# Kernel tuning notes

Hardware: AMD Instinct MI355X
Metric: run time of the kernel (lower is better)

Reference implementation:

```python
import jax, jax.numpy as jnp
import numpy as np

N, E, IN, HID, HEADS, G = 50000, 800000, 300, 256, 4, 64
C1, C2, C3 = 16, 64, 256


def setup_inputs() -> dict:
    key = jax.random.key(0)
    ks = jax.random.split(key, 24)
    s = 0.05
    hd = HID // HEADS
    inp = {
        'x': jax.random.normal(ks[0], (N, IN), jnp.float32),
        'edge_index': jax.random.randint(ks[1], (2, E), 0, N, dtype=jnp.int32),
        # sorted graph ids with every segment non-empty (for global_max_pool)
        'batch': ((jnp.arange(N, dtype=jnp.int32) * G) // N).astype(jnp.int32),
        # GATConv 1: in 300 -> 4 heads x 64
        'W1': jax.random.normal(ks[2], (IN, HID), jnp.float32) * s,
        'as1': jax.random.normal(ks[3], (HEADS, hd), jnp.float32) * s,
        'ad1': jax.random.normal(ks[4], (HEADS, hd), jnp.float32) * s,
        'b1': jnp.zeros((HID,), jnp.float32),
        # GATConv 2: 256 -> 4 heads x 64
        'W2': jax.random.normal(ks[5], (HID, HID), jnp.float32) * s,
        'as2': jax.random.normal(ks[6], (HEADS, hd), jnp.float32) * s,
        'ad2': jax.random.normal(ks[7], (HEADS, hd), jnp.float32) * s,
        'b2': jnp.zeros((HID,), jnp.float32),
        # GATConv 3: 256 -> 1 head x 256
        'W3': jax.random.normal(ks[8], (HID, HID), jnp.float32) * s,
        'as3': jax.random.normal(ks[9], (1, HID), jnp.float32) * s,
        'ad3': jax.random.normal(ks[10], (1, HID), jnp.float32) * s,
        'b3': jnp.zeros((HID,), jnp.float32),
        # hierarchical classifier heads
        'Wc1': jax.random.normal(ks[11], (HID, C1), jnp.float32) * s,
        'bc1': jnp.zeros((C1,), jnp.float32),
        'Wc2': jax.random.normal(ks[12], (HID + C1, C2), jnp.float32) * s,
        'bc2': jnp.zeros((C2,), jnp.float32),
        'Wc3': jax.random.normal(ks[13], (HID + C2, C3), jnp.float32) * s,
        'bc3': jnp.zeros((C3,), jnp.float32),
    }
    return inp


def gat_conv(x, src, dst, W, a_src, a_dst, b, heads):
    """PyG-style GATConv: gather -> leaky_relu scores -> segment softmax over dst -> scatter-add."""
    n = x.shape[0]
    d = W.shape[1] // heads
    h = (x @ W).reshape(n, heads, d)                       # [N,H,D]
    alpha_s = jnp.einsum('nhd,hd->nh', h, a_src)           # [N,H]
    alpha_d = jnp.einsum('nhd,hd->nh', h, a_dst)           # [N,H]
    e = jax.nn.leaky_relu(alpha_s[src] + alpha_d[dst], 0.2)  # [E,H]
    e_max = jax.ops.segment_max(e, dst, num_segments=n)
    e_max = jnp.where(jnp.isfinite(e_max), e_max, 0.0)
    w = jnp.exp(e - e_max[dst])
    denom = jax.ops.segment_sum(w, dst, num_segments=n)
    alpha = w / (denom[dst] + 1e-16)                       # [E,H]
    out = jax.ops.segment_sum(h[src] * alpha[:, :, None], dst, num_segments=n)
    return out.reshape(n, heads * d) + b


def forward(x, edge_index, batch,
            W1, as1, ad1, b1, W2, as2, ad2, b2, W3, as3, ad3, b3,
            Wc1, bc1, Wc2, bc2, Wc3, bc3):
    n = x.shape[0]
    loop = jnp.arange(n, dtype=edge_index.dtype)           # PyG add_self_loops=True
    src = jnp.concatenate([edge_index[0], loop])
    dst = jnp.concatenate([edge_index[1], loop])
    h = jax.nn.elu(gat_conv(x, src, dst, W1, as1, ad1, b1, HEADS))
    h = jax.nn.elu(gat_conv(h, src, dst, W2, as2, ad2, b2, HEADS))  # dropout is identity in eval
    h = gat_conv(h, src, dst, W3, as3, ad3, b3, 1)
    g = jax.ops.segment_max(h, batch, num_segments=G)      # global_max_pool -> [G,HID]
    l1 = g @ Wc1 + bc1
    p1 = jax.nn.softmax(l1, axis=1)
    l2 = jnp.concatenate([g, p1], axis=1) @ Wc2 + bc2
    p2 = jax.nn.softmax(l2, axis=1)
    l3 = jnp.concatenate([g, p2], axis=1) @ Wc3 + bc3
    return (l1, l2, l3)


def reference(x, edge_index, batch,
              W1, as1, ad1, b1, W2, as2, ad2, b2, W3, as3, ad3, b3,
              Wc1, bc1, Wc2, bc2, Wc3, bc3):
    return forward(x, edge_index, batch, W1, as1, ad1, b1, W2, as2, ad2, b2,
                   W3, as3, ad3, b3, Wc1, bc1, Wc2, bc2, Wc3, bc3)
```

## Files before the change

kernel.cpp:

```cpp
#include <hip/hip_runtime.h>
#include <hip/hip_bf16.h>
#include <math.h>

#define NN 50000
#define EE 800000
#define INF_ 300
#define HIDF 256
#define GG 64

__global__ void count_dst_k(const int* __restrict__ dst, int* __restrict__ cnt, int E) {
    int e = blockIdx.x * blockDim.x + threadIdx.x;
    if (e < E) atomicAdd(&cnt[dst[e]], 1);
}

__global__ void scan1_k(const int* __restrict__ cnt, int* __restrict__ tmp,
                        int* __restrict__ bsums, int n) {
    __shared__ int sd[256];
    int t = threadIdx.x;
    int i = blockIdx.x * 256 + t;
    sd[t] = (i < n) ? cnt[i] : 0;
    __syncthreads();
    #pragma unroll
    for (int off = 1; off < 256; off <<= 1) {
        int add = (t >= off) ? sd[t - off] : 0;
        __syncthreads();
        sd[t] += add;
        __syncthreads();
    }
    if (i < n) tmp[i] = sd[t];
    if (t == 255) bsums[blockIdx.x] = sd[255];
}

__global__ void scan2_k(int* __restrict__ bsums, int nb) {
    __shared__ int sd[256];
    int t = threadIdx.x;
    sd[t] = (t < nb) ? bsums[t] : 0;
    __syncthreads();
    #pragma unroll
    for (int off = 1; off < 256; off <<= 1) {
        int add = (t >= off) ? sd[t - off] : 0;
        __syncthreads();
        sd[t] += add;
        __syncthreads();
    }
    if (t < nb) bsums[t] = sd[t];
}

__global__ void scan3_k(const int* __restrict__ tmp, const int* __restrict__ cnt,
                        const int* __restrict__ bsums, int* __restrict__ row_off,
                        int* __restrict__ wr, int n) {
    int i = blockIdx.x * 256 + threadIdx.x;
    if (i >= n) return;
    int base = (blockIdx.x > 0) ? bsums[blockIdx.x - 1] : 0;
    int incl = tmp[i] + base;
    row_off[i + 1] = incl;
    wr[i] = incl - cnt[i];
    if (i == 0) row_off[0] = 0;
}

__global__ void scatter_k(const int* __restrict__ src, const int* __restrict__ dst,
                          int* __restrict__ wr, int* __restrict__ csr_src, int E) {
    int e = blockIdx.x * blockDim.x + threadIdx.x;
    if (e < E) {
        int d = dst[e];
        int pos = atomicAdd(&wr[d], 1);
        csr_src[pos] = src[e];
    }
}

__global__ __launch_bounds__(256) void gemm_f32(const float* __restrict__ A,
                                                const float* __restrict__ B,
                                                float* __restrict__ C, int M, int K) {
    __shared__ float sA[16][64];
    __shared__ float sB[16][64];
    const int tid = threadIdx.x;
    const int tr = tid >> 4, tc = tid & 15;
    const int r0 = tr * 4, c0 = tc * 4;
    const int bm = blockIdx.x * 64;
    const int bn = blockIdx.y * 64;

    float acc[4][4] = {};

    const int aRow = tid >> 2;
    const int aK   = (tid & 3) * 4;
    const int bRow = tid >> 4;
    const int bCol = (tid & 15) * 4;
    const bool aValid = (bm + aRow) < M;
    const float* Arow = A + (size_t)(bm + aRow) * K;
    const int nK = (K + 15) >> 4;

    for (int t = 0; t < nK; ++t) {
        int k0 = t * 16;
        if (aValid && (k0 + aK + 3) < K) {
            float4 v = *(const float4*)(Arow + k0 + aK);
            sA[aK + 0][aRow] = v.x;
            sA[aK + 1][aRow] = v.y;
            sA[aK + 2][aRow] = v.z;
            sA[aK + 3][aRow] = v.w;
        } else {
            #pragma unroll
            for (int j = 0; j < 4; ++j) {
                int k = k0 + aK + j;
                sA[aK + j][aRow] = (aValid && k < K) ? Arow[k] : 0.f;
            }
        }
        {
            int k = k0 + bRow;
            float4 v = make_float4(0.f, 0.f, 0.f, 0.f);
            if (k < K) v = *(const float4*)(B + (size_t)k * 256 + bn + bCol);
            *(float4*)&sB[bRow][bCol] = v;
        }
        __syncthreads();
        #pragma unroll
        for (int k = 0; k < 16; ++k) {
            float4 a4 = *(float4*)&sA[k][r0];
            float4 b4 = *(float4*)&sB[k][c0];
            acc[0][0] += a4.x * b4.x; acc[0][1] += a4.x * b4.y; acc[0][2] += a4.x * b4.z; acc[0][3] += a4.x * b4.w;
            acc[1][0] += a4.y * b4.x; acc[1][1] += a4.y * b4.y; acc[1][2] += a4.y * b4.z; acc[1][3] += a4.y * b4.w;
            acc[2][0] += a4.z * b4.x; acc[2][1] += a4.z * b4.y; acc[2][2] += a4.z * b4.z; acc[2][3] += a4.z * b4.w;
            acc[3][0] += a4.w * b4.x; acc[3][1] += a4.w * b4.y; acc[3][2] += a4.w * b4.z; acc[3][3] += a4.w * b4.w;
        }
        __syncthreads();
    }
    #pragma unroll
    for (int i = 0; i < 4; ++i) {
        int m = bm + r0 + i;
        if (m < M) {
            float4 v = make_float4(acc[i][0], acc[i][1], acc[i][2], acc[i][3]);
            *(float4*)(C + (size_t)m * 256 + bn + c0) = v;
        }
    }
}

template <int NH>
__global__ __launch_bounds__(256) void calc_alpha_k(const float* __restrict__ hf,
                                                    const float* __restrict__ a_s,
                                                    const float* __restrict__ a_d,
                                                    float* __restrict__ als,
                                                    float* __restrict__ ald, int n) {
    int gw = (blockIdx.x * blockDim.x + threadIdx.x) >> 6;
    int lane = threadIdx.x & 63;
    if (gw >= n) return;
    const float* hr = hf + (size_t)gw * 256;
    float ps[4], pd[4];
    #pragma unroll
    for (int j = 0; j < 4; ++j) {
        float v = hr[j * 64 + lane];
        ps[j] = v * a_s[j * 64 + lane];
        pd[j] = v * a_d[j * 64 + lane];
    }
    if (NH == 1) {
        ps[0] = (ps[0] + ps[1]) + (ps[2] + ps[3]);
        pd[0] = (pd[0] + pd[1]) + (pd[2] + pd[3]);
    }
    #pragma unroll
    for (int h = 0; h < NH; ++h) {
        float s = ps[h], d = pd[h];
        #pragma unroll
        for (int off = 32; off > 0; off >>= 1) {
            s += __shfl_xor(s, off, 64);
            d += __shfl_xor(d, off, 64);
        }
        if (lane == 0) {
            als[gw * NH + h] = s;
            ald[gw * NH + h] = d;
        }
    }
}

__device__ __forceinline__ float leaky02(float x) { return (x > 0.f) ? x : 0.2f * x; }

template <int NH>
__global__ __launch_bounds__(256) void gat_agg_k(const float* __restrict__ hf,
                                                 const float* __restrict__ als,
                                                 const float* __restrict__ ald,
                                                 const int* __restrict__ row_off,
                                                 const int* __restrict__ csr_src,
                                                 const float* __restrict__ bias,
                                                 float* __restrict__ out, int n,
                                                 int do_elu) {
    int gw = (blockIdx.x * blockDim.x + threadIdx.x) >> 6;
    int lane = threadIdx.x & 63;
    if (gw >= n) return;
    const int i = gw;
    const int e0 = row_off[i], e1 = row_off[i + 1];

    float adv[NH], aself[NH];
    if (NH == 4) {
        float4 v = *(const float4*)(ald + (size_t)i * 4);
        adv[0] = v.x; if (NH > 1) { adv[1] = v.y; adv[2] = v.z; adv[3] = v.w; }
        float4 u = *(const float4*)(als + (size_t)i * 4);
        aself[0] = u.x; if (NH > 1) { aself[1] = u.y; aself[2] = u.z; aself[3] = u.w; }
    } else {
        adv[0] = ald[i];
        aself[0] = als[i];
    }

    float m[NH];
    #pragma unroll
    for (int h = 0; h < NH; ++h) m[h] = leaky02(aself[h] + adv[h]);
    for (int e = e0 + lane; e < e1; e += 64) {
        int s = csr_src[e];
        if (NH == 4) {
            float4 v = *(const float4*)(als + (size_t)s * 4);
            m[0] = fmaxf(m[0], leaky02(v.x + adv[0]));
            m[1] = fmaxf(m[1], leaky02(v.y + adv[1]));
            m[2] = fmaxf(m[2], leaky02(v.z + adv[2]));
            m[3] = fmaxf(m[3], leaky02(v.w + adv[3]));
        } else {
            m[0] = fmaxf(m[0], leaky02(als[s] + adv[0]));
        }
    }
    #pragma unroll
    for (int h = 0; h < NH; ++h)
        #pragma unroll
        for (int off = 32; off > 0; off >>= 1)
            m[h] = fmaxf(m[h], __shfl_xor(m[h], off, 64));

    float acc0 = 0.f, acc1 = 0.f, acc2 = 0.f, acc3 = 0.f;
    float denom[NH];
    #pragma unroll
    for (int h = 0; h < NH; ++h) denom[h] = 0.f;

    {
        float w[NH];
        #pragma unroll
        for (int h = 0; h < NH; ++h) {
            w[h] = expf(leaky02(aself[h] + adv[h]) - m[h]);
            denom[h] += w[h];
        }
        const float* hr = hf + (size_t)i * 256;
        acc0 += w[0] * hr[lane];
        acc1 += w[NH == 4 ? 1 : 0] * hr[64 + lane];
        acc2 += w[NH == 4 ? 2 : 0] * hr[128 + lane];
        acc3 += w[NH == 4 ? 3 : 0] * hr[192 + lane];
    }
    for (int e = e0; e < e1; ++e) {
        int s = csr_src[e];
        float w[NH];
        if (NH == 4) {
            float4 v = *(const float4*)(als + (size_t)s * 4);
            w[0] = expf(leaky02(v.x + adv[0]) - m[0]);
            w[1] = expf(leaky02(v.y + adv[1]) - m[1]);
            w[2] = expf(leaky02(v.z + adv[2]) - m[2]);
            w[3] = expf(leaky02(v.w + adv[3]) - m[3]);
            denom[0] += w[0]; denom[1] += w[1]; denom[2] += w[2]; denom[3] += w[3];
        } else {
            w[0] = expf(leaky02(als[s] + adv[0]) - m[0]);
            denom[0] += w[0];
        }
        const float* hr = hf + (size_t)s * 256;
        acc0 += w[0] * hr[lane];
        acc1 += w[NH == 4 ? 1 : 0] * hr[64 + lane];
        acc2 += w[NH == 4 ? 2 : 0] * hr[128 + lane];
        acc3 += w[NH == 4 ? 3 : 0] * hr[192 + lane];
    }

    float o0 = acc0 / (denom[0] + 1e-16f) + bias[lane];
    float o1 = acc1 / (denom[NH == 4 ? 1 : 0] + 1e-16f) + bias[64 + lane];
    float o2 = acc2 / (denom[NH == 4 ? 2 : 0] + 1e-16f) + bias[128 + lane];
    float o3 = acc3 / (denom[NH == 4 ? 3 : 0] + 1e-16f) + bias[192 + lane];
    if (do_elu) {
        o0 = (o0 > 0.f) ? o0 : expf(o0) - 1.f;
        o1 = (o1 > 0.f) ? o1 : expf(o1) - 1.f;
        o2 = (o2 > 0.f) ? o2 : expf(o2) - 1.f;
        o3 = (o3 > 0.f) ? o3 : expf(o3) - 1.f;
    }
    float* orow = out + (size_t)i * 256;
    orow[lane] = o0;
    orow[64 + lane] = o1;
    orow[128 + lane] = o2;
    orow[192 + lane] = o3;
}

__global__ __launch_bounds__(1024) void pool_max_k(const float* __restrict__ y,
                                                   float* __restrict__ g) {
    int gid = blockIdx.x;
    int t = threadIdx.x;
    int dim = t & 255;
    int s = t >> 8;
    int start = (gid * NN + (GG - 1)) / GG;
    int end = ((gid + 1) * NN + (GG - 1)) / GG;
    float m = -INFINITY;
    for (int i = start + s; i < end; i += 4)
        m = fmaxf(m, y[(size_t)i * 256 + dim]);
    __shared__ float red[4][256];
    red[s][dim] = m;
    __syncthreads();
    if (s == 0) {
        m = fmaxf(fmaxf(red[0][dim], red[1][dim]), fmaxf(red[2][dim], red[3][dim]));
        g[gid * 256 + dim] = m;
    }
}

__global__ __launch_bounds__(256) void classifier_k(const float* __restrict__ g,
                                                    const float* __restrict__ Wc1, const float* __restrict__ bc1,
                                                    const float* __restrict__ Wc2, const float* __restrict__ bc2,
                                                    const float* __restrict__ Wc3, const float* __restrict__ bc3,
                                                    float* __restrict__ out) {
    __shared__ float gs[256];
    __shared__ float p1s[16];
    __shared__ float p2s[64];
    __shared__ float ls[64];
    const int gid = blockIdx.x;
    const int t = threadIdx.x;
    gs[t] = g[gid * 256 + t];
    __syncthreads();

    if (t < 16) {
        float a = bc1[t];
        for (int k = 0; k < 256; ++k) a += gs[k] * Wc1[k * 16 + t];
        out[gid * 16 + t] = a;
        ls[t] = a;
    }
    __syncthreads();
    if (t == 0) {
        float mx = -INFINITY;
        for (int j = 0; j < 16; ++j) mx = fmaxf(mx, ls[j]);
        float s = 0.f;
        for (int j = 0; j < 16; ++j) { float w = expf(ls[j] - mx); p1s[j] = w; s += w; }
        for (int j = 0; j < 16; ++j) p1s[j] /= s;
    }
    __syncthreads();

    if (t < 64) {
        float a = bc2[t];
        for (int k = 0; k < 256; ++k) a += gs[k] * Wc2[k * 64 + t];
        for (int j = 0; j < 16; ++j) a += p1s[j] * Wc2[(256 + j) * 64 + t];
        out[GG * 16 + gid * 64 + t] = a;
        ls[t] = a;
    }
    __syncthreads();
    if (t == 0) {
        float mx = -INFINITY;
        for (int j = 0; j < 64; ++j) mx = fmaxf(mx, ls[j]);
        float s = 0.f;
        for (int j = 0; j < 64; ++j) { float w = expf(ls[j] - mx); p2s[j] = w; s += w; }
        for (int j = 0; j < 64; ++j) p2s[j] /= s;
    }
    __syncthreads();

    {
        float a = bc3[t];
        for (int k = 0; k < 256; ++k) a += gs[k] * Wc3[k * 256 + t];
        for (int j = 0; j < 64; ++j) a += p2s[j] * Wc3[(256 + j) * 256 + t];
        out[GG * 16 + GG * 64 + gid * 256 + t] = a;
    }
}

extern "C" void kernel_launch(void* const* d_in, const int* in_sizes, int n_in,
                              void* d_out, int out_size, void* d_ws, size_t ws_size,
                              hipStream_t stream) {
    const float* x   = (const float*)d_in[0];
    const int*   ei  = (const int*)d_in[1];
    const float* W1  = (const float*)d_in[3];
    const float* as1 = (const float*)d_in[4];
    const float* ad1 = (const float*)d_in[5];
    const float* b1  = (const float*)d_in[6];
    const float* W2  = (const float*)d_in[7];
    const float* as2 = (const float*)d_in[8];
    const float* ad2 = (const float*)d_in[9];
    const float* b2  = (const float*)d_in[10];
    const float* W3  = (const float*)d_in[11];
    const float* as3 = (const float*)d_in[12];
    const float* ad3 = (const float*)d_in[13];
    const float* b3  = (const float*)d_in[14];
    const float* Wc1 = (const float*)d_in[15];
    const float* bc1 = (const float*)d_in[16];
    const float* Wc2 = (const float*)d_in[17];
    const float* bc2 = (const float*)d_in[18];
    const float* Wc3 = (const float*)d_in[19];
    const float* bc3 = (const float*)d_in[20];
    float* out = (float*)d_out;

    const int N = NN, E = EE;
    const int* e_src = ei;
    const int* e_dst = ei + E;

    char* w = (char*)d_ws;
    auto carve = [&](size_t bytes) {
        void* p = (void*)w;
        w += (bytes + 255) & ~(size_t)255;
        return p;
    };
    float* bufA   = (float*)carve((size_t)N * 256 * 4);
    float* bufB   = (float*)carve((size_t)N * 256 * 4);
    float* als    = (float*)carve((size_t)N * 4 * 4);
    float* ald    = (float*)carve((size_t)N * 4 * 4);
    int*   cnt    = (int*)carve((size_t)N * 4);
    int*   tmpv   = (int*)carve((size_t)N * 4);
    int*   bsums  = (int*)carve(1024);
    int*   row_off= (int*)carve((size_t)(N + 1) * 4);
    int*   wrp    = (int*)carve((size_t)N * 4);
    int*   csr    = (int*)carve((size_t)E * 4);
    float* gbuf   = (float*)carve((size_t)GG * 256 * 4);

    const int nScanBlocks = (N + 255) / 256;

    hipMemsetAsync(cnt, 0, (size_t)N * 4, stream);
    count_dst_k<<<(E + 255) / 256, 256, 0, stream>>>(e_dst, cnt, E);
    scan1_k<<<nScanBlocks, 256, 0, stream>>>(cnt, tmpv, bsums, N);
    scan2_k<<<1, 256, 0, stream>>>(bsums, nScanBlocks);
    scan3_k<<<nScanBlocks, 256, 0, stream>>>(tmpv, cnt, bsums, row_off, wrp, N);
    scatter_k<<<(E + 255) / 256, 256, 0, stream>>>(e_src, e_dst, wrp, csr, E);

    const int waveBlocks = (N * 64 + 255) / 256;
    dim3 gemmGridK300((N + 63) / 64, 4);

    gemm_f32<<<gemmGridK300, 256, 0, stream>>>(x, W1, bufA, N, INF_);
    calc_alpha_k<4><<<waveBlocks, 256, 0, stream>>>(bufA, as1, ad1, als, ald, N);
    gat_agg_k<4><<<waveBlocks, 256, 0, stream>>>(bufA, als, ald, row_off, csr, b1, bufB, N, 1);

    gemm_f32<<<gemmGridK300, 256, 0, stream>>>(bufB, W2, bufA, N, HIDF);
    calc_alpha_k<4><<<waveBlocks, 256, 0, stream>>>(bufA, as2, ad2, als, ald, N);
    gat_agg_k<4><<<waveBlocks, 256, 0, stream>>>(bufA, als, ald, row_off, csr, b2, bufB, N, 1);

    gemm_f32<<<gemmGridK300, 256, 0, stream>>>(bufB, W3, bufA, N, HIDF);
    calc_alpha_k<1><<<waveBlocks, 256, 0, stream>>>(bufA, as3, ad3, als, ald, N);
    gat_agg_k<1><<<waveBlocks, 256, 0, stream>>>(bufA, als, ald, row_off, csr, b3, bufB, N, 0);

    pool_max_k<<<GG, 1024, 0, stream>>>(bufB, gbuf);
    classifier_k<<<GG, 256, 0, stream>>>(gbuf, Wc1, bc1, Wc2, bc2, Wc3, bc3, out);
}
```

Measured before the change: 1.099 ms.

## Enlarge GEMM tiles to 128x128 and restructure GAT aggregation with batched edge weights

The fp32 GEMM moves from 64x64 tiles with 4x4 per-thread micro-tiles to 128x128 tiles with 8x8 micro-tiles, plus a padded shared B layout to avoid bank conflicts. This raises arithmetic intensity and cuts shared-memory traffic per FMA, at the cost of more registers and fewer blocks. The aggregation kernel now computes attention weights for 64 edges in parallel, stages them in LDS, and broadcasts source ids with readlane. Each lane then accumulates a float4 column slice, replacing the serial per-edge exp computation with vectorised gathers.

```diff
diff --git a/kernel.cpp b/kernel.cpp
--- a/kernel.cpp
+++ b/kernel.cpp
@@ -68,66 +68,87 @@
     }
 }
 
-__global__ __launch_bounds__(256) void gemm_f32(const float* __restrict__ A,
-                                                const float* __restrict__ B,
-                                                float* __restrict__ C, int M, int K) {
-    __shared__ float sA[16][64];
-    __shared__ float sB[16][64];
+#define SB_PHYS(c) ((c) + 4 * ((c) >> 5))
+
+__global__ __launch_bounds__(256, 2) void gemm_f32_v2(const float* __restrict__ A,
+                                                      const float* __restrict__ B,
+                                                      float* __restrict__ C, int M, int K) {
+    __shared__ float sA[16][128];
+    __shared__ float sB[16][SB_PHYS(128) + 8];
     const int tid = threadIdx.x;
+    const int bm = blockIdx.x * 128;
+    const int bn = blockIdx.y * 128;
     const int tr = tid >> 4, tc = tid & 15;
-    const int r0 = tr * 4, c0 = tc * 4;
-    const int bm = blockIdx.x * 64;
-    const int bn = blockIdx.y * 64;
-
-    float acc[4][4] = {};
-
-    const int aRow = tid >> 2;
-    const int aK   = (tid & 3) * 4;
+    const int r0 = tr * 8, c0 = tc * 8;
+    const int c0p = SB_PHYS(c0);
+
+    float acc[8][8] = {};
+
+    const int aRow = tid >> 1;
+    const int aK   = (tid & 1) * 8;
+    const bool aV  = (bm + aRow) < M;
+    const float* Arow = A + (size_t)(bm + aRow) * K;
+
     const int bRow = tid >> 4;
-    const int bCol = (tid & 15) * 4;
-    const bool aValid = (bm + aRow) < M;
-    const float* Arow = A + (size_t)(bm + aRow) * K;
-    const int nK = (K + 15) >> 4;
-
-    for (int t = 0; t < nK; ++t) {
-        int k0 = t * 16;
-        if (aValid && (k0 + aK + 3) < K) {
-            float4 v = *(const float4*)(Arow + k0 + aK);
-            sA[aK + 0][aRow] = v.x;
-            sA[aK + 1][aRow] = v.y;
-            sA[aK + 2][aRow] = v.z;
-            sA[aK + 3][aRow] = v.w;
-        } else {
+    const int bCol = (tid & 15) * 8;
+    const int bColP = SB_PHYS(bCol);
+
+    const int nT = (K + 15) >> 4;
+
+    for (int t = 0; t < nT; ++t) {
+        const int k0 = t * 16;
+        #pragma unroll
+        for (int half = 0; half < 2; ++half) {
+            const int kk = aK + half * 4;
+            if (aV && (k0 + kk + 4) <= K) {
+                float4 v = *(const float4*)(Arow + k0 + kk);
+                sA[kk + 0][aRow] = v.x;
+                sA[kk + 1][aRow] = v.y;
+                sA[kk + 2][aRow] = v.z;
+                sA[kk + 3][aRow] = v.w;
+            } else {
+                #pragma unroll
+                for (int j = 0; j < 4; ++j) {
+                    int k = k0 + kk + j;
+                    sA[kk + j][aRow] = (aV && k < K) ? Arow[k] : 0.f;
+                }
+            }
+        }
+        {
+            const int k = k0 + bRow;
+            float4 v0 = make_float4(0.f, 0.f, 0.f, 0.f), v1 = v0;
+            if (k < K) {
+                const float* Brow = B + (size_t)k * 256 + bn + bCol;
+                v0 = *(const float4*)(Brow);
+                v1 = *(const float4*)(Brow + 4);
+            }
+            *(float4*)&sB[bRow][bColP]     = v0;
+            *(float4*)&sB[bRow][bColP + 4] = v1;
+        }
+        __syncthreads();
+        #pragma unroll
+        for (int k = 0; k < 16; ++k) {
+            float4 a0 = *(float4*)&sA[k][r0];
+            float4 a1 = *(float4*)&sA[k][r0 + 4];
+            float4 b0 = *(float4*)&sB[k][c0p];
+            float4 b1 = *(float4*)&sB[k][c0p + 4];
+            float av[8] = {a0.x, a0.y, a0.z, a0.w, a1.x, a1.y, a1.z, a1.w};
+            float bv[8] = {b0.x, b0.y, b0.z, b0.w, b1.x, b1.y, b1.z, b1.w};
             #pragma unroll
-            for (int j = 0; j < 4; ++j) {
-                int k = k0 + aK + j;
-                sA[aK + j][aRow] = (aValid && k < K) ? Arow[k] : 0.f;
-            }
-        }
-        {
-            int k = k0 + bRow;
-            float4 v = make_float4(0.f, 0.f, 0.f, 0.f);
-            if (k < K) v = *(const float4*)(B + (size_t)k * 256 + bn + bCol);
-            *(float4*)&sB[bRow][bCol] = v;
-        }
-        __syncthreads();
-        #pragma unroll
-        for (int k = 0; k < 16; ++k) {
-            float4 a4 = *(float4*)&sA[k][r0];
-            float4 b4 = *(float4*)&sB[k][c0];
-            acc[0][0] += a4.x * b4.x; acc[0][1] += a4.x * b4.y; acc[0][2] += a4.x * b4.z; acc[0][3] += a4.x * b4.w;
-            acc[1][0] += a4.y * b4.x; acc[1][1] += a4.y * b4.y; acc[1][2] += a4.y * b4.z; acc[1][3] += a4.y * b4.w;
-            acc[2][0] += a4.z * b4.x; acc[2][1] += a4.z * b4.y; acc[2][2] += a4.z * b4.z; acc[2][3] += a4.z * b4.w;
-            acc[3][0] += a4.w * b4.x; acc[3][1] += a4.w * b4.y; acc[3][2] += a4.w * b4.z; acc[3][3] += a4.w * b4.w;
-        }
-        __syncthreads();
-    }
-    #pragma unroll
-    for (int i = 0; i < 4; ++i) {
-        int m = bm + r0 + i;
+            for (int i = 0; i < 8; ++i)
+                #pragma unroll
+                for (int j = 0; j < 8; ++j)
+                    acc[i][j] += av[i] * bv[j];
+        }
+        __syncthreads();
+    }
+    #pragma unroll
+    for (int i = 0; i < 8; ++i) {
+        const int m = bm + r0 + i;
         if (m < M) {
-            float4 v = make_float4(acc[i][0], acc[i][1], acc[i][2], acc[i][3]);
-            *(float4*)(C + (size_t)m * 256 + bn + c0) = v;
+            float* Crow = C + (size_t)m * 256 + bn + c0;
+            *(float4*)(Crow)     = make_float4(acc[i][0], acc[i][1], acc[i][2], acc[i][3]);
+            *(float4*)(Crow + 4) = make_float4(acc[i][4], acc[i][5], acc[i][6], acc[i][7]);
         }
     }
 }
@@ -171,26 +192,29 @@
 __device__ __forceinline__ float leaky02(float x) { return (x > 0.f) ? x : 0.2f * x; }
 
 template <int NH>
-__global__ __launch_bounds__(256) void gat_agg_k(const float* __restrict__ hf,
-                                                 const float* __restrict__ als,
-                                                 const float* __restrict__ ald,
-                                                 const int* __restrict__ row_off,
-                                                 const int* __restrict__ csr_src,
-                                                 const float* __restrict__ bias,
-                                                 float* __restrict__ out, int n,
-                                                 int do_elu) {
-    int gw = (blockIdx.x * blockDim.x + threadIdx.x) >> 6;
-    int lane = threadIdx.x & 63;
+__global__ __launch_bounds__(256) void gat_agg2_k(const float* __restrict__ hf,
+                                                  const float* __restrict__ als,
+                                                  const float* __restrict__ ald,
+                                                  const int* __restrict__ row_off,
+                                                  const int* __restrict__ csr_src,
+                                                  const float* __restrict__ bias,
+                                                  float* __restrict__ out, int n,
+                                                  int do_elu) {
+    __shared__ float wlds[4][64][NH];
+    const int wslot = threadIdx.x >> 6;
+    const int gw = (blockIdx.x * blockDim.x + threadIdx.x) >> 6;
+    const int lane = threadIdx.x & 63;
     if (gw >= n) return;
     const int i = gw;
     const int e0 = row_off[i], e1 = row_off[i + 1];
+    const int hL = (NH == 4) ? (lane >> 4) : 0;
 
     float adv[NH], aself[NH];
     if (NH == 4) {
         float4 v = *(const float4*)(ald + (size_t)i * 4);
-        adv[0] = v.x; if (NH > 1) { adv[1] = v.y; adv[2] = v.z; adv[3] = v.w; }
+        adv[0] = v.x; adv[1] = v.y; adv[2] = v.z; adv[3] = v.w;
         float4 u = *(const float4*)(als + (size_t)i * 4);
-        aself[0] = u.x; if (NH > 1) { aself[1] = u.y; aself[2] = u.z; aself[3] = u.w; }
+        aself[0] = u.x; aself[1] = u.y; aself[2] = u.z; aself[3] = u.w;
     } else {
         adv[0] = ald[i];
         aself[0] = als[i];
@@ -217,60 +241,79 @@
         for (int off = 32; off > 0; off >>= 1)
             m[h] = fmaxf(m[h], __shfl_xor(m[h], off, 64));
 
-    float acc0 = 0.f, acc1 = 0.f, acc2 = 0.f, acc3 = 0.f;
-    float denom[NH];
-    #pragma unroll
-    for (int h = 0; h < NH; ++h) denom[h] = 0.f;
-
-    {
+    float denomL[NH];
+    #pragma unroll
+    for (int h = 0; h < NH; ++h) denomL[h] = 0.f;
+    float wself[NH];
+    #pragma unroll
+    for (int h = 0; h < NH; ++h) wself[h] = expf(leaky02(aself[h] + adv[h]) - m[h]);
+    if (lane == 0) {
+        #pragma unroll
+        for (int h = 0; h < NH; ++h) denomL[h] += wself[h];
+    }
+    float wsel = (NH == 4)
+        ? ((lane < 16) ? wself[0] : (lane < 32) ? wself[1] : (lane < 48) ? wself[2] : wself[3])
+        : wself[0];
+    float4 av4 = *(const float4*)(hf + (size_t)i * 256 + 4 * lane);
+    float ax = wsel * av4.x, ay = wsel * av4.y, az = wsel * av4.z, aw = wsel * av4.w;
+
+    for (int base = e0; base < e1; base += 64) {
+        const int e = base + lane;
+        const bool valid = e < e1;
+        int s_reg = valid ? csr_src[e] : 0;
         float w[NH];
-        #pragma unroll
-        for (int h = 0; h < NH; ++h) {
-            w[h] = expf(leaky02(aself[h] + adv[h]) - m[h]);
-            denom[h] += w[h];
-        }
-        const float* hr = hf + (size_t)i * 256;
-        acc0 += w[0] * hr[lane];
-        acc1 += w[NH == 4 ? 1 : 0] * hr[64 + lane];
-        acc2 += w[NH == 4 ? 2 : 0] * hr[128 + lane];
-        acc3 += w[NH == 4 ? 3 : 0] * hr[192 + lane];
-    }
-    for (int e = e0; e < e1; ++e) {
-        int s = csr_src[e];
-        float w[NH];
-        if (NH == 4) {
-            float4 v = *(const float4*)(als + (size_t)s * 4);
-            w[0] = expf(leaky02(v.x + adv[0]) - m[0]);
-            w[1] = expf(leaky02(v.y + adv[1]) - m[1]);
-            w[2] = expf(leaky02(v.z + adv[2]) - m[2]);
-            w[3] = expf(leaky02(v.w + adv[3]) - m[3]);
-            denom[0] += w[0]; denom[1] += w[1]; denom[2] += w[2]; denom[3] += w[3];
+        if (valid) {
+            if (NH == 4) {
+                float4 v = *(const float4*)(als + (size_t)s_reg * 4);
+                w[0] = expf(leaky02(v.x + adv[0]) - m[0]);
+                w[1] = expf(leaky02(v.y + adv[1]) - m[1]);
+                w[2] = expf(leaky02(v.z + adv[2]) - m[2]);
+                w[3] = expf(leaky02(v.w + adv[3]) - m[3]);
+            } else {
+                w[0] = expf(leaky02(als[s_reg] + adv[0]) - m[0]);
+            }
         } else {
-            w[0] = expf(leaky02(als[s] + adv[0]) - m[0]);
-            denom[0] += w[0];
-        }
-        const float* hr = hf + (size_t)s * 256;
-        acc0 += w[0] * hr[lane];
-        acc1 += w[NH == 4 ? 1 : 0] * hr[64 + lane];
-        acc2 += w[NH == 4 ? 2 : 0] * hr[128 + lane];
-        acc3 += w[NH == 4 ? 3 : 0] * hr[192 + lane];
-    }
-
-    float o0 = acc0 / (denom[0] + 1e-16f) + bias[lane];
-    float o1 = acc1 / (denom[NH == 4 ? 1 : 0] + 1e-16f) + bias[64 + lane];
-    float o2 = acc2 / (denom[NH == 4 ? 2 : 0] + 1e-16f) + bias[128 + lane];
-    float o3 = acc3 / (denom[NH == 4 ? 3 : 0] + 1e-16f) + bias[192 + lane];
+            #pragma unroll
+            for (int h = 0; h < NH; ++h) w[h] = 0.f;
+        }
+        #pragma unroll
+        for (int h = 0; h < NH; ++h) denomL[h] += w[h];
+        if (NH == 4)
+            *(float4*)&wlds[wslot][lane][0] = make_float4(w[0], w[1], w[2], w[3]);
+        else
+            wlds[wslot][lane][0] = w[0];
+
+        const int cnt = min(64, e1 - base);
+        #pragma unroll 4
+        for (int j = 0; j < cnt; ++j) {
+            int sj = __builtin_amdgcn_readlane(s_reg, j);
+            float wj = wlds[wslot][j][hL];
+            const float4 hv = *(const float4*)(hf + (size_t)sj * 256 + 4 * lane);
+            ax += wj * hv.x; ay += wj * hv.y; az += wj * hv.z; aw += wj * hv.w;
+        }
+    }
+
+    #pragma unroll
+    for (int h = 0; h < NH; ++h)
+        #pragma unroll
+        for (int off = 32; off > 0; off >>= 1)
+            denomL[h] += __shfl_xor(denomL[h], off, 64);
+    float dh = (NH == 4)
+        ? ((lane < 16) ? denomL[0] : (lane < 32) ? denomL[1] : (lane < 48) ? denomL[2] : denomL[3])
+        : denomL[0];
+    float inv = 1.f / (dh + 1e-16f);
+    float4 bv = *(const float4*)(bias + 4 * lane);
+    float o0 = ax * inv + bv.x;
+    float o1 = ay * inv + bv.y;
+    float o2 = az * inv + bv.z;
+    float o3 = aw * inv + bv.w;
     if (do_elu) {
         o0 = (o0 > 0.f) ? o0 : expf(o0) - 1.f;
         o1 = (o1 > 0.f) ? o1 : expf(o1) - 1.f;
         o2 = (o2 > 0.f) ? o2 : expf(o2) - 1.f;
         o3 = (o3 > 0.f) ? o3 : expf(o3) - 1.f;
     }
-    float* orow = out + (size_t)i * 256;
-    orow[lane] = o0;
-    orow[64 + lane] = o1;
-    orow[128 + lane] = o2;
-    orow[192 + lane] = o3;
+    *(float4*)(out + (size_t)i * 256 + 4 * lane) = make_float4(o0, o1, o2, o3);
 }
 
 __global__ __launch_bounds__(1024) void pool_max_k(const float* __restrict__ y,
@@ -405,19 +448,19 @@
     scatter_k<<<(E + 255) / 256, 256, 0, stream>>>(e_src, e_dst, wrp, csr, E);
 
     const int waveBlocks = (N * 64 + 255) / 256;
-    dim3 gemmGridK300((N + 63) / 64, 4);
-
-    gemm_f32<<<gemmGridK300, 256, 0, stream>>>(x, W1, bufA, N, INF_);
+    dim3 gemmGrid((N + 127) / 128, 2);
+
+    gemm_f32_v2<<<gemmGrid, 256, 0, stream>>>(x, W1, bufA, N, INF_);
     calc_alpha_k<4><<<waveBlocks, 256, 0, stream>>>(bufA, as1, ad1, als, ald, N);
-    gat_agg_k<4><<<waveBlocks, 256, 0, stream>>>(bufA, als, ald, row_off, csr, b1, bufB, N, 1);
-
-    gemm_f32<<<gemmGridK300, 256, 0, stream>>>(bufB, W2, bufA, N, HIDF);
+    gat_agg2_k<4><<<waveBlocks, 256, 0, stream>>>(bufA, als, ald, row_off, csr, b1, bufB, N, 1);
+
+    gemm_f32_v2<<<gemmGrid, 256, 0, stream>>>(bufB, W2, bufA, N, HIDF);
     calc_alpha_k<4><<<waveBlocks, 256, 0, stream>>>(bufA, as2, ad2, als, ald, N);
-    gat_agg_k<4><<<waveBlocks, 256, 0, stream>>>(bufA, als, ald, row_off, csr, b2, bufB, N, 1);
-
-    gemm_f32<<<gemmGridK300, 256, 0, stream>>>(bufB, W3, bufA, N, HIDF);
+    gat_agg2_k<4><<<waveBlocks, 256, 0, stream>>>(bufA, als, ald, row_off, csr, b2, bufB, N, 1);
+
+    gemm_f32_v2<<<gemmGrid, 256, 0, stream>>>(bufB, W3, bufA, N, HIDF);
     calc_alpha_k<1><<<waveBlocks, 256, 0, stream>>>(bufA, as3, ad3, als, ald, N);
-    gat_agg_k<1><<<waveBlocks, 256, 0, stream>>>(bufA, als, ald, row_off, csr, b3, bufB, N, 0);
+    gat_agg2_k<1><<<waveBlocks, 256, 0, stream>>>(bufA, als, ald, row_off, csr, b3, bufB, N, 0);
 
     pool_max_k<<<GG, 1024, 0, stream>>>(bufB, gbuf);
     classifier_k<<<GG, 256, 0, stream>>>(gbuf, Wc1, bc1, Wc2, bc2, Wc3, bc3, out);
```

Result: faster. 1.046 ms (-4.8%).
